# Kernel tuning notes

Measured on AMD Instinct MI355X. Metric: run time of the kernel, lower is better.

## Reference

```python
import jax, jax.numpy as jnp
import numpy as np

NEG_INF = -1e9
HIDDEN = 1024
HEADS = 16
SPH = HIDDEN // HEADS  # 64
B, Q, M = 8, 512, 512
R = Q + M


def rel_shift(x):
    # x: [N, H, Q, R] -> TransformerXL relative shift
    N, H, Qd, Rd = x.shape
    x = jnp.pad(x, ((0, 0), (0, 0), (0, 0), (1, 0)))
    x = x.reshape(N, H, Rd + 1, Qd)
    return x[:, :, 1:, :].reshape(N, H, Qd, Rd)


def setup_inputs() -> dict:
    key = jax.random.key(0)
    ks = jax.random.split(key, 11)
    std = 1.0 / np.sqrt(HIDDEN)
    # causal token mask: query position i (global pos M+i) may attend to ref pos j <= M+i
    q_pos = jnp.arange(Q)[:, None] + M
    r_pos = jnp.arange(R)[None, :]
    token_mask = (r_pos > q_pos).astype(jnp.float32)[None, None]  # [1,1,Q,R]
    return {
        "query_seqs": jax.random.normal(ks[0], (B, Q, HIDDEN), jnp.float32),
        "memory_seqs": jax.random.normal(ks[1], (B, M, HIDDEN), jnp.float32),
        "positional_encoding": jax.random.normal(ks[2], (R, HIDDEN), jnp.float32),
        "token_mask": token_mask,
        "content_bias": jax.random.normal(ks[3], (HEADS, SPH), jnp.float32) * 0.02,
        "position_bias": jax.random.normal(ks[4], (HEADS, SPH), jnp.float32) * 0.02,
        "Wq": jax.random.normal(ks[5], (HIDDEN, HEADS, SPH), jnp.float32) * std,
        "Wkc": jax.random.normal(ks[6], (HIDDEN, HEADS, SPH), jnp.float32) * std,
        "Wkp": jax.random.normal(ks[7], (HIDDEN, HEADS, SPH), jnp.float32) * std,
        "Wv": jax.random.normal(ks[8], (HIDDEN, HEADS, SPH), jnp.float32) * std,
        "Wo": jax.random.normal(ks[9], (HEADS, SPH, HIDDEN), jnp.float32) * std,
    }


def reference(query_seqs, memory_seqs, positional_encoding, token_mask,
              content_bias, position_bias, Wq, Wkc, Wkp, Wv, Wo):
    reference_seqs = jnp.concatenate([memory_seqs, query_seqs], axis=1)  # [B,R,D]
    query = jnp.einsum('nqd,dhs->nqhs', query_seqs, Wq)            # [B,Q,H,S]
    key_content = jnp.einsum('nrd,dhs->nrhs', reference_seqs, Wkc)  # [B,R,H,S]
    key_position = jnp.einsum('rd,dhs->rhs', positional_encoding, Wkp)  # [R,H,S]
    value = jnp.einsum('nrd,dhs->nrhs', reference_seqs, Wv)         # [B,R,H,S]

    content = jnp.einsum('nqhs,nrhs->nhqr', query + content_bias, key_content)
    positions = jnp.einsum('nqhs,rhs->nhqr', query + position_bias, key_position)
    positions = rel_shift(positions)

    scores = (content + positions) / np.sqrt(SPH) + token_mask * NEG_INF
    attn = jax.nn.softmax(scores, axis=3)  # [B,H,Q,R]
    out = jnp.einsum('nhqr,nrhs->nqhs', attn, value)
    return jnp.einsum('nqhs,hsd->nqd', out, Wo)  # [B,Q,D]
```

## Files before the change

### kernel.cpp

```cpp
#include <hip/hip_runtime.h>

#define B_ 8
#define Q_ 512
#define M_ 512
#define R_ 1024
#define H_ 16
#define S_ 64
#define D_ 1024
#define MEG 1048576L

typedef unsigned short ushort_t;
typedef __attribute__((ext_vector_type(8))) _Float16 f16x8;
typedef __attribute__((ext_vector_type(8))) unsigned short u16x8;
typedef __attribute__((ext_vector_type(4))) unsigned short u16x4;
typedef __attribute__((ext_vector_type(4))) float f32x4;
typedef __attribute__((ext_vector_type(2))) unsigned int u32x2;

__device__ __forceinline__ unsigned short h2u(_Float16 h) {
    union { _Float16 h; unsigned short u; } v; v.h = h; return v.u;
}
__device__ __forceinline__ unsigned int pk_f16(float a, float b) {
    union { _Float16 h[2]; unsigned int u; } v;
    v.h[0] = (_Float16)a; v.h[1] = (_Float16)b; return v.u;
}
__device__ __forceinline__ void async_cp16(const ushort_t* g, ushort_t* l) {
    __builtin_amdgcn_global_load_lds(
        (const __attribute__((address_space(1))) void*)g,
        (__attribute__((address_space(3))) void*)l, 16, 0, 0);
}

__global__ __launch_bounds__(256) void zero_out_f32_k(float* __restrict__ p, int n) {
    int i = blockIdx.x * 256 + threadIdx.x;
    if (i < n) p[i] = 0.f;
}

__global__ __launch_bounds__(256) void prep_k(
    const float* __restrict__ mem, const float* __restrict__ qry,
    const float* __restrict__ pos, const float* __restrict__ cb,
    const float* __restrict__ pb,
    const float* __restrict__ Wkc, const float* __restrict__ Wv,
    const float* __restrict__ Wkp, const float* __restrict__ Wq,
    const float* __restrict__ Wo,
    ushort_t* __restrict__ qcat, ushort_t* __restrict__ posb,
    ushort_t* __restrict__ cbpb, ushort_t* __restrict__ BT4,
    ushort_t* __restrict__ WoT) {
    int x = blockIdx.x, y = blockIdx.y, t = threadIdx.x;
    if (y < 5) {
        const float* in; ushort_t* out;
        switch (y) {
            case 0: in = Wkc; out = BT4;           break;
            case 1: in = Wv;  out = BT4 + MEG;     break;
            case 2: in = Wkp; out = BT4 + 2 * MEG; break;
            case 3: in = Wq;  out = BT4 + 3 * MEG; break;
            default: in = Wo; out = WoT;           break;
        }
        __shared__ ushort_t tile[32][33];
        int bx = (x & 31) * 32, by = (x >> 5) * 32;
        int tx = t & 31, ty = t >> 5;
        #pragma unroll
        for (int i = 0; i < 32; i += 8)
            tile[ty + i][tx] = h2u((_Float16)in[(long)(by + ty + i) * 1024 + bx + tx]);
        __syncthreads();
        #pragma unroll
        for (int i = 0; i < 32; i += 8)
            out[(long)(bx + ty + i) * 1024 + by + tx] = tile[tx][ty + i];
    } else if (y < 13) {
        int g = y - 5, r = x;
        const float* src = (r < 512) ? (mem + ((long)g * 512 + r) * 1024)
                                     : (qry + ((long)g * 512 + (r - 512)) * 1024);
        ushort_t* dst = qcat + ((long)g * 1024 + r) * 1024;
        int i = t * 4;
        f32x4 v = *(const f32x4*)(src + i);
        u32x2 o; o[0] = pk_f16(v[0], v[1]); o[1] = pk_f16(v[2], v[3]);
        *(u32x2*)(dst + i) = o;
    } else if (y == 13) {
        int i = t * 4;
        f32x4 v = *(const f32x4*)(pos + (long)x * 1024 + i);
        u32x2 o; o[0] = pk_f16(v[0], v[1]); o[1] = pk_f16(v[2], v[3]);
        *(u32x2*)(posb + (long)x * 1024 + i) = o;
    } else {
        if (x == 0) {
            for (int i = t; i < 1024; i += 256) {
                cbpb[i]        = h2u((_Float16)cb[i]);
                cbpb[1024 + i] = h2u((_Float16)pb[i]);
            }
        }
    }
}

__device__ __forceinline__ void gemm_body(const ushort_t* Arow0,
                                          const ushort_t* BTrow0,
                                          void* Crow0, long crs, int mode) {
    __shared__ __align__(16) ushort_t Al[2][128 * 32];
    __shared__ __align__(16) ushort_t Bl[2][128 * 32];

    int t = threadIdx.x;
    int wave = t >> 6, lane = t & 63, quad = lane >> 4, l16 = lane & 15;
    int wm = (wave & 1) * 64, wn = (wave >> 1) * 64;

    f32x4 acc[4][4];
    #pragma unroll
    for (int im = 0; im < 4; ++im)
        #pragma unroll
        for (int in = 0; in < 4; ++in) acc[im][in] = (f32x4){0.f, 0.f, 0.f, 0.f};

    int grow = lane >> 2, gcol = (lane & 3) * 8;
    const ushort_t* ga0 = Arow0 + (long)(wave * 32 + grow) * 1024 + gcol;
    const ushort_t* ga1 = Arow0 + (long)(wave * 32 + 16 + grow) * 1024 + gcol;
    const ushort_t* gb0 = BTrow0 + (long)(wave * 32 + grow) * 1024 + gcol;
    const ushort_t* gb1 = BTrow0 + (long)(wave * 32 + 16 + grow) * 1024 + gcol;
    int lo0 = (wave * 2 + 0) * 512;
    int lo1 = (wave * 2 + 1) * 512;

    async_cp16(ga0, &Al[0][lo0]);
    async_cp16(ga1, &Al[0][lo1]);
    async_cp16(gb0, &Bl[0][lo0]);
    async_cp16(gb1, &Bl[0][lo1]);
    __syncthreads();

    int cur = 0;
    for (int k0 = 0; k0 < 1024; k0 += 32) {
        int nxt = cur ^ 1;
        if (k0 + 32 < 1024) {
            async_cp16(ga0 + k0 + 32, &Al[nxt][lo0]);
            async_cp16(ga1 + k0 + 32, &Al[nxt][lo1]);
            async_cp16(gb0 + k0 + 32, &Bl[nxt][lo0]);
            async_cp16(gb1 + k0 + 32, &Bl[nxt][lo1]);
        }

        f16x8 af[4], bf[4];
        #pragma unroll
        for (int im = 0; im < 4; ++im)
            af[im] = *(const f16x8*)&Al[cur][(wm + im * 16 + l16) * 32 + quad * 8];
        #pragma unroll
        for (int in = 0; in < 4; ++in)
            bf[in] = *(const f16x8*)&Bl[cur][(wn + in * 16 + l16) * 32 + quad * 8];
        __builtin_amdgcn_s_setprio(1);
        #pragma unroll
        for (int im = 0; im < 4; ++im)
            #pragma unroll
            for (int in = 0; in < 4; ++in)
                acc[im][in] = __builtin_amdgcn_mfma_f32_16x16x32_f16(
                    af[im], bf[in], acc[im][in], 0, 0, 0);
        __builtin_amdgcn_s_setprio(0);
        __syncthreads();
        cur = nxt;
    }

    if (mode == 2) {
        #pragma unroll
        for (int im = 0; im < 4; ++im)
            #pragma unroll
            for (int in = 0; in < 4; ++in) {
                u16x4 pk;
                #pragma unroll
                for (int reg = 0; reg < 4; ++reg) pk[reg] = h2u((_Float16)acc[im][in][reg]);
                long addr = (long)(wn + in * 16 + l16) * 1024 + wm + im * 16 + quad * 4;
                *(u16x4*)((ushort_t*)Crow0 + addr) = pk;
            }
        return;
    }
    #pragma unroll
    for (int im = 0; im < 4; ++im)
        #pragma unroll
        for (int in = 0; in < 4; ++in)
            #pragma unroll
            for (int reg = 0; reg < 4; ++reg) {
                long addr = (long)(wm + im * 16 + quad * 4 + reg) * crs
                          + wn + in * 16 + l16;
                if (mode == 1) ((float*)Crow0)[addr] = acc[im][in][reg];
                else ((ushort_t*)Crow0)[addr] = h2u((_Float16)acc[im][in][reg]);
            }
}

__global__ __launch_bounds__(256) void gemm_mega(
    const ushort_t* __restrict__ qcat, const ushort_t* __restrict__ posb,
    const ushort_t* __restrict__ BT4,
    ushort_t* __restrict__ kcC, ushort_t* __restrict__ vT,
    ushort_t* __restrict__ qproj, ushort_t* __restrict__ kpp) {
    int id = blockIdx.x;
    if (id < 1024) {
        int z = id >> 7, tl = id & 127;
        int x = tl >> 4, y = tl & 15;
        const ushort_t* Arow0 = qcat + (long)z * MEG + (long)x * 128 * 1024;
        if (y < 8) {
            gemm_body(Arow0, BT4 + (long)y * 128 * 1024,
                      kcC + (long)z * MEG + (long)x * 128 * 1024 + y * 128, 1024, 0);
        } else {
            int n0 = (y - 8) * 128;
            gemm_body(Arow0, BT4 + (long)(1024 + n0) * 1024,
                      vT + ((long)z * 1024 + n0) * 1024 + x * 128, 0, 2);
        }
    } else if (id < 1088) {
        int u = id - 1024;
        int x = u >> 3, y = u & 7;
        gemm_body(posb + (long)x * 128 * 1024,
                  BT4 + (long)(2048 + y * 128) * 1024,
                  kpp + (long)x * 128 * 1024 + y * 128, 1024, 0);
    } else {
        int u = id - 1088;
        int b = u >> 5, v2 = u & 31;
        int x = v2 >> 3, y = v2 & 7;
        gemm_body(qcat + (long)b * MEG + (long)(512 + x * 128) * 1024,
                  BT4 + (long)(3072 + y * 128) * 1024,
                  qproj + (long)b * 512 * 1024 + (long)x * 128 * 1024 + y * 128, 1024, 0);
    }
}

__global__ __launch_bounds__(256) void gemm_fin(
    const ushort_t* __restrict__ A, const ushort_t* __restrict__ WoT,
    float* __restrict__ out) {
    gemm_body(A + (long)blockIdx.x * 128 * 1024,
              WoT + (long)blockIdx.y * 128 * 1024,
              out + (long)blockIdx.x * 128 * 1024 + blockIdx.y * 128, 1024, 1);
}

__global__ __launch_bounds__(512) void attn_kernel(
    const ushort_t* __restrict__ qproj,
    const ushort_t* __restrict__ kc,
    const ushort_t* __restrict__ kp,
    const ushort_t* __restrict__ vT,
    const ushort_t* __restrict__ cbpb,
    ushort_t* __restrict__ aout)
{
    int qt = (blockIdx.x + ((blockIdx.y >> 6) << 1)) & 3;
    int q0 = qt * 128;
    int bh = blockIdx.y;
    int b = bh >> 4, h = bh & 15;
    int t = threadIdx.x;
    int wave = t >> 6, lane = t & 63, quad = lane >> 4, l16 = lane & 15;

    __shared__ __align__(16) ushort_t Kc[64][72];
    __shared__ __align__(16) ushort_t Vt[64][72];
    __shared__ __align__(16) ushort_t Kp[192][72];
    __shared__ __align__(16) char Pu[8][2304];
    ushort_t* Pl = (ushort_t*)&Pu[wave][0];

    const ushort_t* qrow = qproj + ((long)(b * Q_ + q0 + wave * 16 + l16)) * 1024 + h * 64;
    f16x8 qcf[2], qpf[2];
    #pragma unroll
    for (int ks = 0; ks < 2; ++ks) {
        f16x8 qv  = *(const f16x8*)(qrow + ks * 32 + quad * 8);
        f16x8 cbv = *(const f16x8*)(cbpb + h * 64 + ks * 32 + quad * 8);
        f16x8 pbv = *(const f16x8*)(cbpb + 1024 + h * 64 + ks * 32 + quad * 8);
        qcf[ks] = qv + cbv;
        qpf[ks] = qv + pbv;
    }

    float m_s[4];
    f32x4 o_acc[4], ls4;
    #pragma unroll
    for (int r = 0; r < 4; ++r) {
        m_s[r] = -1e30f;
        o_acc[r] = (f32x4){0.f, 0.f, 0.f, 0.f};
    }
    ls4 = (f32x4){0.f, 0.f, 0.f, 0.f};

    f16x8 ones;
    #pragma unroll
    for (int j = 0; j < 8; ++j) ones[j] = (_Float16)1.0f;

    int srow = t >> 3, sc0 = (t & 7) * 8;
    const ushort_t* kcb = kc + ((long)(b * R_) + srow) * 1024 + h * 64 + sc0;
    const ushort_t* vtb = vT + ((long)(b * 1024 + h * 64 + srow)) * 1024 + sc0;
    const ushort_t* kpb = kp + h * 64 + sc0;

    int ntiles = ((q0 + 639) >> 6) + 1;

    u16x8 rKc = *(const u16x8*)(kcb);
    u16x8 rVt = *(const u16x8*)(vtb);
    u16x8 rKp[3];
    {
        int jb0 = 384 - q0;
        #pragma unroll
        for (int p = 0; p < 3; ++p) {
            int j = jb0 + p * 64 + srow;
            int jc = j > 1023 ? 1023 : j;
            rKp[p] = *(const u16x8*)(kpb + (long)jc * 1024);
        }
    }

    for (int it = 0; it < ntiles; ++it) {
        int r0 = it * 64;
        int jbase = r0 - q0 + 384;
        int gb0 = jbase >> 4;
        __syncthreads();
        *(u16x8*)&Kc[srow][sc0] = rKc;
        *(u16x8*)&Vt[srow][sc0] = rVt;
        if (it == 0) {
            #pragma unroll
            for (int p = 0; p < 3; ++p) {
                int j = jbase + p * 64 + srow;
                int ph = ((j >> 4) % 12) * 16 + (j & 15);
                *(u16x8*)&Kp[ph][sc0] = rKp[p];
            }
        } else {
            int j = jbase + 128 + srow;
            int ph = ((j >> 4) % 12) * 16 + (j & 15);
            *(u16x8*)&Kp[ph][sc0] = rKp[0];
        }
        __syncthreads();
        if (it + 1 < ntiles) {
            int r1 = r0 + 64;
            rKc = *(const u16x8*)(kcb + (long)r1 * 1024);
            rVt = *(const u16x8*)(vtb + r1);
            int j = r1 - q0 + 512 + srow;
            int jc = j > 1023 ? 1023 : j;
            rKp[0] = *(const u16x8*)(kpb + (long)jc * 1024);
        }

        f32x4 sc[4];
        #pragma unroll
        for (int s = 0; s < 4; ++s) sc[s] = (f32x4){0.f, 0.f, 0.f, 0.f};
        f32x4 dd[5];
        #pragma unroll
        for (int s = 0; s < 5; ++s) dd[s] = (f32x4){0.f, 0.f, 0.f, 0.f};

        __builtin_amdgcn_s_setprio(1);
        #pragma unroll
        for (int ks = 0; ks < 2; ++ks)
            #pragma unroll
            for (int sub = 0; sub < 4; ++sub) {
                f16x8 bb = *(const f16x8*)&Kc[sub * 16 + l16][ks * 32 + quad * 8];
                sc[sub] = __builtin_amdgcn_mfma_f32_16x16x32_f16(qcf[ks], bb, sc[sub], 0, 0, 0);
            }
        #pragma unroll
        for (int ks = 0; ks < 2; ++ks)
            #pragma unroll
            for (int sub = 0; sub < 5; ++sub) {
                int pb = (gb0 + 7 - wave + sub) % 12;
                f16x8 bb = *(const f16x8*)&Kp[pb * 16 + l16][ks * 32 + quad * 8];
                dd[sub] = __builtin_amdgcn_mfma_f32_16x16x32_f16(qpf[ks], bb, dd[sub], 0, 0, 0);
            }
        __builtin_amdgcn_s_setprio(0);

        #pragma unroll
        for (int reg = 0; reg < 4; ++reg) {
            int row16 = quad * 4 + reg;
            int src = (lane & 48) + ((l16 + 15 - row16) & 15);
            float dsh[5];
            #pragma unroll
            for (int sub = 0; sub < 5; ++sub)
                dsh[sub] = __shfl(dd[sub][reg], src);
            #pragma unroll
            for (int sub = 0; sub < 4; ++sub) {
                float dval = (l16 > row16) ? dsh[sub + 1] : dsh[sub];
                float sv = (sc[sub][reg] + dval) * 0.125f;
                int rl = sub * 16 + l16;
                if (r0 + rl > q0 + wave * 16 + row16 + 512) sv = -1e30f;
                sc[sub][reg] = sv;
            }
        }

        float vmax[4];
        #pragma unroll
        for (int reg = 0; reg < 4; ++reg)
            vmax[reg] = fmaxf(fmaxf(sc[0][reg], sc[1][reg]),
                              fmaxf(sc[2][reg], sc[3][reg]));
        int ok = (vmax[0] <= m_s[0] + 8.f) & (vmax[1] <= m_s[1] + 8.f) &
                 (vmax[2] <= m_s[2] + 8.f) & (vmax[3] <= m_s[3] + 8.f);
        if (!__all(ok)) {
            #pragma unroll
            for (int reg = 0; reg < 4; ++reg) {
                float rm = vmax[reg];
                #pragma unroll
                for (int m = 1; m < 16; m <<= 1) rm = fmaxf(rm, __shfl_xor(rm, m));
                float mn = fmaxf(m_s[reg], rm);
                float alpha = __expf(m_s[reg] - mn);
                m_s[reg] = mn;
                ls4[reg] *= alpha;
                #pragma unroll
                for (int sub = 0; sub < 4; ++sub)
                    o_acc[sub][reg] *= alpha;
            }
        }
        #pragma unroll
        for (int sub = 0; sub < 4; ++sub)
            #pragma unroll
            for (int reg = 0; reg < 4; ++reg) {
                float p = __expf(sc[sub][reg] - m_s[reg]);
                Pl[(quad * 4 + reg) * 72 + sub * 16 + l16] = h2u((_Float16)p);
            }

        f16x8 a0 = *(const f16x8*)&Pl[l16 * 72 + quad * 8];
        f16x8 a1 = *(const f16x8*)&Pl[l16 * 72 + 32 + quad * 8];
        __builtin_amdgcn_s_setprio(1);
        ls4 = __builtin_amdgcn_mfma_f32_16x16x32_f16(a0, ones, ls4, 0, 0, 0);
        ls4 = __builtin_amdgcn_mfma_f32_16x16x32_f16(a1, ones, ls4, 0, 0, 0);
        #pragma unroll
        for (int sub = 0; sub < 4; ++sub) {
            f16x8 bb0 = *(const f16x8*)&Vt[sub * 16 + l16][quad * 8];
            o_acc[sub] = __builtin_amdgcn_mfma_f32_16x16x32_f16(a0, bb0, o_acc[sub], 0, 0, 0);
            f16x8 bb1 = *(const f16x8*)&Vt[sub * 16 + l16][32 + quad * 8];
            o_acc[sub] = __builtin_amdgcn_mfma_f32_16x16x32_f16(a1, bb1, o_acc[sub], 0, 0, 0);
        }
        __builtin_amdgcn_s_setprio(0);
    }

    #pragma unroll
    for (int reg = 0; reg < 4; ++reg) {
        float inv = 1.f / ls4[reg];
        int qg = q0 + wave * 16 + quad * 4 + reg;
        ushort_t* orow = aout + ((long)(b * Q_ + qg)) * 1024 + h * 64;
        #pragma unroll
        for (int sub = 0; sub < 4; ++sub)
            orow[sub * 16 + l16] = h2u((_Float16)(o_acc[sub][reg] * inv));
    }
}

extern "C" void kernel_launch(void* const* d_in, const int* in_sizes, int n_in,
                              void* d_out, int out_size, void* d_ws, size_t ws_size,
                              hipStream_t stream) {
    const float* query  = (const float*)d_in[0];
    const float* memory = (const float*)d_in[1];
    const float* pos    = (const float*)d_in[2];
    const float* cb  = (const float*)d_in[4];
    const float* pb  = (const float*)d_in[5];
    const float* Wq  = (const float*)d_in[6];
    const float* Wkc = (const float*)d_in[7];
    const float* Wkp = (const float*)d_in[8];
    const float* Wv  = (const float*)d_in[9];
    const float* Wo  = (const float*)d_in[10];
    float* out = (float*)d_out;
    ushort_t* ws = (ushort_t*)d_ws;

    size_t ws_elems = ws_size / 2;
    if (ws_elems < 36 * MEG) {
        zero_out_f32_k<<<(out_size + 255) / 256, 256, 0, stream>>>(out, out_size);
        return;
    }

    ushort_t* cbpb  = ws;
    ushort_t* BT4   = ws + MEG;
    ushort_t* WoT   = BT4 + 4 * MEG;
    ushort_t* kpp   = WoT + MEG;
    ushort_t* posb  = kpp + MEG;
    ushort_t* qproj = posb + MEG;
    ushort_t* kcC   = qproj + 4 * MEG;
    ushort_t* vT    = kcC + 8 * MEG;
    ushort_t* qcat  = vT + 8 * MEG;
    ushort_t* aout  = qproj;

    prep_k<<<dim3(1024, 15), 256, 0, stream>>>(
        memory, query, pos, cb, pb, Wkc, Wv, Wkp, Wq, Wo,
        qcat, posb, cbpb, BT4, WoT);
    gemm_mega<<<dim3(1344), 256, 0, stream>>>(qcat, posb, BT4, kcC, vT, qproj, kpp);
    attn_kernel<<<dim3(4, 128), 512, 0, stream>>>(qproj, kcC, kpp, vT, cbpb, aout);
    gemm_fin<<<dim3(32, 8, 1), 256, 0, stream>>>(aout, WoT, out);
}
```

Before: 245.0 us.

## Triple-buffer GEMM LDS tiles with explicit vmcnt waits and single barrier

Changes the projection GEMM mainloop from double-buffered to triple-buffered LDS staging. Loads are issued two k-steps ahead, and partial s_waitcnt vmcnt(4) lets the next tile's copies stay in flight while the current tile is consumed. This replaces the two __syncthreads per iteration with one barrier per iteration. It raises LDS use per block, which may lower occupancy, and relies on hand-counted vmcnt values being correct.

```diff
diff --git a/kernel.cpp b/kernel.cpp
--- a/kernel.cpp
+++ b/kernel.cpp
@@ -91,8 +91,8 @@
 __device__ __forceinline__ void gemm_body(const ushort_t* Arow0,
                                           const ushort_t* BTrow0,
                                           void* Crow0, long crs, int mode) {
-    __shared__ __align__(16) ushort_t Al[2][128 * 32];
-    __shared__ __align__(16) ushort_t Bl[2][128 * 32];
+    __shared__ __align__(16) ushort_t Al[3][128 * 32];
+    __shared__ __align__(16) ushort_t Bl[3][128 * 32];
 
     int t = threadIdx.x;
     int wave = t >> 6, lane = t & 63, quad = lane >> 4, l16 = lane & 15;
@@ -112,29 +112,31 @@
     int lo0 = (wave * 2 + 0) * 512;
     int lo1 = (wave * 2 + 1) * 512;
 
-    async_cp16(ga0, &Al[0][lo0]);
-    async_cp16(ga1, &Al[0][lo1]);
-    async_cp16(gb0, &Bl[0][lo0]);
-    async_cp16(gb1, &Bl[0][lo1]);
-    __syncthreads();
-
-    int cur = 0;
-    for (int k0 = 0; k0 < 1024; k0 += 32) {
-        int nxt = cur ^ 1;
-        if (k0 + 32 < 1024) {
-            async_cp16(ga0 + k0 + 32, &Al[nxt][lo0]);
-            async_cp16(ga1 + k0 + 32, &Al[nxt][lo1]);
-            async_cp16(gb0 + k0 + 32, &Bl[nxt][lo0]);
-            async_cp16(gb1 + k0 + 32, &Bl[nxt][lo1]);
-        }
-
+    #define STAGE_(buf, kst) do {                          \
+        int k0_ = (kst) * 32;                              \
+        async_cp16(ga0 + k0_, &Al[buf][lo0]);              \
+        async_cp16(ga1 + k0_, &Al[buf][lo1]);              \
+        async_cp16(gb0 + k0_, &Bl[buf][lo0]);              \
+        async_cp16(gb1 + k0_, &Bl[buf][lo1]);              \
+    } while (0)
+
+    STAGE_(0, 0);
+    STAGE_(1, 1);
+
+    for (int j = 0; j < 32; ++j) {
+        if (j < 31) asm volatile("s_waitcnt vmcnt(4)" ::: "memory");
+        else        asm volatile("s_waitcnt vmcnt(0)" ::: "memory");
+        __builtin_amdgcn_s_barrier();
+        if (j + 2 < 32) STAGE_((j + 2) % 3, j + 2);
+
+        int cb = j % 3;
         f16x8 af[4], bf[4];
         #pragma unroll
         for (int im = 0; im < 4; ++im)
-            af[im] = *(const f16x8*)&Al[cur][(wm + im * 16 + l16) * 32 + quad * 8];
+            af[im] = *(const f16x8*)&Al[cb][(wm + im * 16 + l16) * 32 + quad * 8];
         #pragma unroll
         for (int in = 0; in < 4; ++in)
-            bf[in] = *(const f16x8*)&Bl[cur][(wn + in * 16 + l16) * 32 + quad * 8];
+            bf[in] = *(const f16x8*)&Bl[cb][(wn + in * 16 + l16) * 32 + quad * 8];
         __builtin_amdgcn_s_setprio(1);
         #pragma unroll
         for (int im = 0; im < 4; ++im)
@@ -143,9 +145,8 @@
                 acc[im][in] = __builtin_amdgcn_mfma_f32_16x16x32_f16(
                     af[im], bf[in], acc[im][in], 0, 0, 0);
         __builtin_amdgcn_s_setprio(0);
-        __syncthreads();
-        cur = nxt;
-    }
+    }
+    #undef STAGE_
 
     if (mode == 2) {
         #pragma unroll
```

After: 252.9 us. +3.2%, slower.

## Triple-buffer GEMM shared tiles with explicit vmcnt waits and one barrier per step

Applied to the files above, without the earlier changes.

Turns the double-buffered LDS pipeline of the projection GEMM into a three-stage ring, prefetching two K-steps ahead. Each step waits with s_waitcnt vmcnt(4), leaving the newest stage's async copies in flight, then issues a single barrier before staging the next tile. The goal is to hide global-load latency better and drop the trailing barrier. It uses 50% more shared memory, which may lower occupancy, and relies on the vmcnt accounting matching the async copy count.

```diff
diff --git a/kernel.cpp b/kernel.cpp
--- a/kernel.cpp
+++ b/kernel.cpp
@@ -91,8 +91,8 @@
 __device__ __forceinline__ void gemm_body(const ushort_t* Arow0,
                                           const ushort_t* BTrow0,
                                           void* Crow0, long crs, int mode) {
-    __shared__ __align__(16) ushort_t Al[2][128 * 32];
-    __shared__ __align__(16) ushort_t Bl[2][128 * 32];
+    __shared__ __align__(16) ushort_t Al[3][128 * 32];
+    __shared__ __align__(16) ushort_t Bl[3][128 * 32];
 
     int t = threadIdx.x;
     int wave = t >> 6, lane = t & 63, quad = lane >> 4, l16 = lane & 15;
@@ -116,36 +116,48 @@
     async_cp16(ga1, &Al[0][lo1]);
     async_cp16(gb0, &Bl[0][lo0]);
     async_cp16(gb1, &Bl[0][lo1]);
-    __syncthreads();
-
-    int cur = 0;
-    for (int k0 = 0; k0 < 1024; k0 += 32) {
-        int nxt = cur ^ 1;
-        if (k0 + 32 < 1024) {
-            async_cp16(ga0 + k0 + 32, &Al[nxt][lo0]);
-            async_cp16(ga1 + k0 + 32, &Al[nxt][lo1]);
-            async_cp16(gb0 + k0 + 32, &Bl[nxt][lo0]);
-            async_cp16(gb1 + k0 + 32, &Bl[nxt][lo1]);
-        }
-
-        f16x8 af[4], bf[4];
-        #pragma unroll
-        for (int im = 0; im < 4; ++im)
-            af[im] = *(const f16x8*)&Al[cur][(wm + im * 16 + l16) * 32 + quad * 8];
-        #pragma unroll
-        for (int in = 0; in < 4; ++in)
-            bf[in] = *(const f16x8*)&Bl[cur][(wn + in * 16 + l16) * 32 + quad * 8];
-        __builtin_amdgcn_s_setprio(1);
-        #pragma unroll
-        for (int im = 0; im < 4; ++im)
-            #pragma unroll
-            for (int in = 0; in < 4; ++in)
-                acc[im][in] = __builtin_amdgcn_mfma_f32_16x16x32_f16(
-                    af[im], bf[in], acc[im][in], 0, 0, 0);
-        __builtin_amdgcn_s_setprio(0);
-        __syncthreads();
-        cur = nxt;
-    }
+    async_cp16(ga0 + 32, &Al[1][lo0]);
+    async_cp16(ga1 + 32, &Al[1][lo1]);
+    async_cp16(gb0 + 32, &Bl[1][lo0]);
+    async_cp16(gb1 + 32, &Bl[1][lo1]);
+
+#define KSTEP(J, CB, NB, WAITSTR, DOSTAGE) do {                               \
+    asm volatile("s_waitcnt vmcnt(" WAITSTR ")" ::: "memory");                \
+    __builtin_amdgcn_s_barrier();                                             \
+    if (DOSTAGE) {                                                            \
+        int k0_ = ((J) + 2) * 32;                                             \
+        async_cp16(ga0 + k0_, &Al[NB][lo0]);                                  \
+        async_cp16(ga1 + k0_, &Al[NB][lo1]);                                  \
+        async_cp16(gb0 + k0_, &Bl[NB][lo0]);                                  \
+        async_cp16(gb1 + k0_, &Bl[NB][lo1]);                                  \
+    }                                                                         \
+    {                                                                         \
+        f16x8 af[4], bf[4];                                                   \
+        _Pragma("unroll")                                                     \
+        for (int im = 0; im < 4; ++im)                                        \
+            af[im] = *(const f16x8*)&Al[CB][(wm + im * 16 + l16) * 32 + quad * 8]; \
+        _Pragma("unroll")                                                     \
+        for (int in = 0; in < 4; ++in)                                        \
+            bf[in] = *(const f16x8*)&Bl[CB][(wn + in * 16 + l16) * 32 + quad * 8]; \
+        __builtin_amdgcn_s_setprio(1);                                        \
+        _Pragma("unroll")                                                     \
+        for (int im = 0; im < 4; ++im)                                        \
+            _Pragma("unroll")                                                 \
+            for (int in = 0; in < 4; ++in)                                    \
+                acc[im][in] = __builtin_amdgcn_mfma_f32_16x16x32_f16(         \
+                    af[im], bf[in], acc[im][in], 0, 0, 0);                    \
+        __builtin_amdgcn_s_setprio(0);                                        \
+    }                                                                         \
+} while (0)
+
+    for (int jj = 0; jj < 30; jj += 3) {
+        KSTEP(jj + 0, 0, 2, "4", true);
+        KSTEP(jj + 1, 1, 0, "4", true);
+        KSTEP(jj + 2, 2, 1, "4", true);
+    }
+    KSTEP(30, 0, 2, "4", false);
+    KSTEP(31, 1, 0, "0", false);
+#undef KSTEP
 
     if (mode == 2) {
         #pragma unroll
```

After: 261.8 us. +6.8%, slower.

## Double GEMM K-tile to 64 with XOR-swizzled LDS layout

Applied to the files above, without the earlier changes.

The shared GEMM body now stages 128x64 K-slices of A and B per buffer instead of 128x32, so each loop iteration runs two MFMA sub-steps and there are half as many barriers and prefetch rounds. The global-to-LDS copy uses a per-row XOR swizzle on the column offset, and the fragment reads apply the matching swizzle to avoid LDS bank conflicts with the wider 64-element rows. LDS use per block doubles, which may reduce occupancy.

```diff
diff --git a/kernel.cpp b/kernel.cpp
--- a/kernel.cpp
+++ b/kernel.cpp
@@ -91,8 +91,8 @@
 __device__ __forceinline__ void gemm_body(const ushort_t* Arow0,
                                           const ushort_t* BTrow0,
                                           void* Crow0, long crs, int mode) {
-    __shared__ __align__(16) ushort_t Al[2][128 * 32];
-    __shared__ __align__(16) ushort_t Bl[2][128 * 32];
+    __shared__ __align__(16) ushort_t Al[2][128 * 64];
+    __shared__ __align__(16) ushort_t Bl[2][128 * 64];
 
     int t = threadIdx.x;
     int wave = t >> 6, lane = t & 63, quad = lane >> 4, l16 = lane & 15;
@@ -104,48 +104,54 @@
         #pragma unroll
         for (int in = 0; in < 4; ++in) acc[im][in] = (f32x4){0.f, 0.f, 0.f, 0.f};
 
-    int grow = lane >> 2, gcol = (lane & 3) * 8;
-    const ushort_t* ga0 = Arow0 + (long)(wave * 32 + grow) * 1024 + gcol;
-    const ushort_t* ga1 = Arow0 + (long)(wave * 32 + 16 + grow) * 1024 + gcol;
-    const ushort_t* gb0 = BTrow0 + (long)(wave * 32 + grow) * 1024 + gcol;
-    const ushort_t* gb1 = BTrow0 + (long)(wave * 32 + 16 + grow) * 1024 + gcol;
-    int lo0 = (wave * 2 + 0) * 512;
-    int lo1 = (wave * 2 + 1) * 512;
-
-    async_cp16(ga0, &Al[0][lo0]);
-    async_cp16(ga1, &Al[0][lo1]);
-    async_cp16(gb0, &Bl[0][lo0]);
-    async_cp16(gb1, &Bl[0][lo1]);
+    int gcol = ((t & 7) * 8) ^ (((t >> 3) & 7) << 3);
+    const ushort_t* gA = Arow0 + (long)(t >> 3) * 1024 + gcol;
+    const ushort_t* gB = BTrow0 + (long)(t >> 3) * 1024 + gcol;
+    int lo = wave * 512;
+
+#define STAGE(BUF, KOFF) do {                                          \
+    async_cp16(gA + 0 * 32768 + (KOFF), &Al[BUF][lo + 0 * 2048]);      \
+    async_cp16(gA + 1 * 32768 + (KOFF), &Al[BUF][lo + 1 * 2048]);      \
+    async_cp16(gA + 2 * 32768 + (KOFF), &Al[BUF][lo + 2 * 2048]);      \
+    async_cp16(gA + 3 * 32768 + (KOFF), &Al[BUF][lo + 3 * 2048]);      \
+    async_cp16(gB + 0 * 32768 + (KOFF), &Bl[BUF][lo + 0 * 2048]);      \
+    async_cp16(gB + 1 * 32768 + (KOFF), &Bl[BUF][lo + 1 * 2048]);      \
+    async_cp16(gB + 2 * 32768 + (KOFF), &Bl[BUF][lo + 2 * 2048]);      \
+    async_cp16(gB + 3 * 32768 + (KOFF), &Bl[BUF][lo + 3 * 2048]);      \
+} while (0)
+
+    STAGE(0, 0);
     __syncthreads();
 
+    int rswz = (l16 & 7) << 3;
     int cur = 0;
-    for (int k0 = 0; k0 < 1024; k0 += 32) {
+    for (int k0 = 0; k0 < 1024; k0 += 64) {
         int nxt = cur ^ 1;
-        if (k0 + 32 < 1024) {
-            async_cp16(ga0 + k0 + 32, &Al[nxt][lo0]);
-            async_cp16(ga1 + k0 + 32, &Al[nxt][lo1]);
-            async_cp16(gb0 + k0 + 32, &Bl[nxt][lo0]);
-            async_cp16(gb1 + k0 + 32, &Bl[nxt][lo1]);
-        }
-
-        f16x8 af[4], bf[4];
-        #pragma unroll
-        for (int im = 0; im < 4; ++im)
-            af[im] = *(const f16x8*)&Al[cur][(wm + im * 16 + l16) * 32 + quad * 8];
-        #pragma unroll
-        for (int in = 0; in < 4; ++in)
-            bf[in] = *(const f16x8*)&Bl[cur][(wn + in * 16 + l16) * 32 + quad * 8];
-        __builtin_amdgcn_s_setprio(1);
-        #pragma unroll
-        for (int im = 0; im < 4; ++im)
+        if (k0 + 64 < 1024) STAGE(nxt, k0 + 64);
+
+        #pragma unroll
+        for (int ks = 0; ks < 2; ++ks) {
+            int rc = (ks * 32 + quad * 8) ^ rswz;
+            f16x8 af[4], bf[4];
+            #pragma unroll
+            for (int im = 0; im < 4; ++im)
+                af[im] = *(const f16x8*)&Al[cur][(wm + im * 16 + l16) * 64 + rc];
             #pragma unroll
             for (int in = 0; in < 4; ++in)
-                acc[im][in] = __builtin_amdgcn_mfma_f32_16x16x32_f16(
-                    af[im], bf[in], acc[im][in], 0, 0, 0);
-        __builtin_amdgcn_s_setprio(0);
+                bf[in] = *(const f16x8*)&Bl[cur][(wn + in * 16 + l16) * 64 + rc];
+            __builtin_amdgcn_s_setprio(1);
+            #pragma unroll
+            for (int im = 0; im < 4; ++im)
+                #pragma unroll
+                for (int in = 0; in < 4; ++in)
+                    acc[im][in] = __builtin_amdgcn_mfma_f32_16x16x32_f16(
+                        af[im], bf[in], acc[im][in], 0, 0, 0);
+            __builtin_amdgcn_s_setprio(0);
+        }
         __syncthreads();
         cur = nxt;
     }
+#undef STAGE
 
     if (mode == 2) {
         #pragma unroll
```

After: 252.4 us. 3.0% more time.
